# Kernel optimization log

Hardware: AMD Instinct MI355X
Metric: run time of the kernel (lower is better)

Reference implementation:

```python
import jax, jax.numpy as jnp
import numpy as np

N_SRC, N_DST, E = 10000, 40000, 1_280_000
IN_DIM, OUT_DIM, FEAT, O_DIM = 128, 64, 64, 300


def setup_inputs() -> dict:
    key = jax.random.key(0)
    ks = jax.random.split(key, 10)
    s = 0.05
    return {
        "h": jax.random.normal(ks[0], (N_SRC, IN_DIM), jnp.float32),
        "o": jax.random.normal(ks[1], (N_DST, O_DIM), jnp.float32),
        "tfidf": jax.random.normal(ks[2], (E, FEAT), jnp.float32),
        "W_fc": jax.random.normal(ks[3], (IN_DIM, OUT_DIM), jnp.float32) * s,
        "W_fc1": jax.random.normal(ks[4], (O_DIM, OUT_DIM), jnp.float32) * s,
        "W_feat": jax.random.normal(ks[5], (FEAT, OUT_DIM), jnp.float32) * s,
        "b_feat": jax.random.normal(ks[6], (OUT_DIM,), jnp.float32) * s,
        "W_attn": jax.random.normal(ks[7], (OUT_DIM, 1), jnp.float32) * s,
        "edge_src": jax.random.randint(ks[8], (E,), 0, N_SRC, jnp.int32),
        "edge_dst": jax.random.randint(ks[9], (E,), 0, N_DST, jnp.int32),
    }


def reference(h, o, tfidf, W_fc, W_fc1, W_feat, b_feat, W_attn, edge_src, edge_dst):
    n_dst = o.shape[0]
    # node projections: z on sentence (src) nodes via fc, on word (dst) nodes via fc1
    z_src = h @ W_fc                      # [N_SRC, D]
    z_dst = o @ W_fc1                     # [N_DST, D]
    # edge attention: z2 = src.z + dst.z + feat_fc(tfidfembed)
    dfeat = tfidf @ W_feat + b_feat       # [E, D]
    z2 = z_src[edge_src] + z_dst[edge_dst] + dfeat
    z3 = jnp.where(z2 > 0, z2, 0.01 * z2)  # leaky_relu, torch default slope
    e = (z3 @ W_attn)[:, 0]               # [E]
    # segment softmax over incoming edges of each dst (word) node
    m = jax.ops.segment_max(e, edge_dst, num_segments=n_dst)   # [N_DST]
    e_exp = jnp.exp(e - m[edge_dst])                           # [E]
    denom = jax.ops.segment_sum(e_exp, edge_dst, num_segments=n_dst)
    alpha = e_exp / jnp.maximum(denom, 1e-9)[edge_dst]         # [E]
    # weighted sum of src z into dst mailbox
    out = jax.ops.segment_sum(alpha[:, None] * z_src[edge_src], edge_dst,
                              num_segments=n_dst)              # [N_DST, D]
    return out
```

## Files before the change

kernel.cpp:

```cpp
#include <hip/hip_runtime.h>
#include <hip/hip_bf16.h>

#define N_SRC 10000
#define N_DST 40000
#define NE    1280000
#define IN_DIM 128
#define O_DIM  300
#define D      64
#define FEAT   64
#define NB     157

typedef __bf16 bf16x8 __attribute__((ext_vector_type(8)));
typedef __bf16 bf16x4 __attribute__((ext_vector_type(4)));
typedef float  f32x4  __attribute__((ext_vector_type(4)));

__global__ __launch_bounds__(256) void k_zsrc(const float* __restrict__ h,
                                              const float* __restrict__ Wfc,
                                              float* __restrict__ z,
                                              __bf16* __restrict__ zh){
    __shared__ float w[IN_DIM * D];
    for (int i = threadIdx.x; i < IN_DIM * D; i += blockDim.x) w[i] = Wfc[i];
    __syncthreads();
    int lane = threadIdx.x & 63;
    int wid  = blockIdx.x * 4 + (threadIdx.x >> 6);
    int nw   = gridDim.x * 4;
    for (int r0 = wid * 4; r0 < N_SRC; r0 += nw * 4){
        const f32x4* p0 = (const f32x4*)(h + (size_t)(r0 + 0) * IN_DIM);
        const f32x4* p1 = (const f32x4*)(h + (size_t)(r0 + 1) * IN_DIM);
        const f32x4* p2 = (const f32x4*)(h + (size_t)(r0 + 2) * IN_DIM);
        const f32x4* p3 = (const f32x4*)(h + (size_t)(r0 + 3) * IN_DIM);
        float a0 = 0.f, a1 = 0.f, a2 = 0.f, a3 = 0.f;
        #pragma unroll 4
        for (int k4 = 0; k4 < IN_DIM / 4; ++k4){
            f32x4 v0 = p0[k4], v1 = p1[k4], v2 = p2[k4], v3 = p3[k4];
            #pragma unroll
            for (int i = 0; i < 4; ++i){
                float wv = w[(k4 * 4 + i) * D + lane];
                a0 += v0[i] * wv; a1 += v1[i] * wv;
                a2 += v2[i] * wv; a3 += v3[i] * wv;
            }
        }
        z[(size_t)(r0 + 0) * D + lane] = a0; zh[(size_t)(r0 + 0) * D + lane] = (__bf16)a0;
        z[(size_t)(r0 + 1) * D + lane] = a1; zh[(size_t)(r0 + 1) * D + lane] = (__bf16)a1;
        z[(size_t)(r0 + 2) * D + lane] = a2; zh[(size_t)(r0 + 2) * D + lane] = (__bf16)a2;
        z[(size_t)(r0 + 3) * D + lane] = a3; zh[(size_t)(r0 + 3) * D + lane] = (__bf16)a3;
    }
}

__global__ __launch_bounds__(256) void k_zdst(const float* __restrict__ o,
                                              const float* __restrict__ Wfc1,
                                              float* __restrict__ z){
    extern __shared__ float w[];
    for (int i = threadIdx.x; i < O_DIM * D; i += blockDim.x) w[i] = Wfc1[i];
    __syncthreads();
    int lane = threadIdx.x & 63;
    int wid  = blockIdx.x * 4 + (threadIdx.x >> 6);
    int nw   = gridDim.x * 4;
    for (int r0 = wid * 4; r0 < N_DST; r0 += nw * 4){
        const f32x4* p0 = (const f32x4*)(o + (size_t)(r0 + 0) * O_DIM);
        const f32x4* p1 = (const f32x4*)(o + (size_t)(r0 + 1) * O_DIM);
        const f32x4* p2 = (const f32x4*)(o + (size_t)(r0 + 2) * O_DIM);
        const f32x4* p3 = (const f32x4*)(o + (size_t)(r0 + 3) * O_DIM);
        float a0 = 0.f, a1 = 0.f, a2 = 0.f, a3 = 0.f;
        #pragma unroll 5
        for (int k4 = 0; k4 < O_DIM / 4; ++k4){
            f32x4 v0 = p0[k4], v1 = p1[k4], v2 = p2[k4], v3 = p3[k4];
            #pragma unroll
            for (int i = 0; i < 4; ++i){
                float wv = w[(k4 * 4 + i) * D + lane];
                a0 += v0[i] * wv; a1 += v1[i] * wv;
                a2 += v2[i] * wv; a3 += v3[i] * wv;
            }
        }
        z[(size_t)(r0 + 0) * D + lane] = a0;
        z[(size_t)(r0 + 1) * D + lane] = a1;
        z[(size_t)(r0 + 2) * D + lane] = a2;
        z[(size_t)(r0 + 3) * D + lane] = a3;
    }
}

__global__ __launch_bounds__(256) void k_rank(const int* __restrict__ edst,
                                              int* __restrict__ cnt,
                                              int* __restrict__ rank){
    int i = blockIdx.x * blockDim.x + threadIdx.x;
    if (i < NE) rank[i] = atomicAdd(&cnt[edst[i]], 1);
}

__device__ __forceinline__ int block_incl_scan(int c, int* wsum){
    int lane = threadIdx.x & 63, w = threadIdx.x >> 6;
    int v = c;
    #pragma unroll
    for (int off = 1; off < 64; off <<= 1){
        int u = __shfl_up(v, off);
        if (lane >= off) v += u;
    }
    if (lane == 63) wsum[w] = v;
    __syncthreads();
    int add = 0;
    for (int ww = 0; ww < w; ++ww) add += wsum[ww];
    return v + add;
}

__global__ __launch_bounds__(256) void k_scan1(const int* __restrict__ cnt,
                                               int* __restrict__ bsum){
    __shared__ int wsum[4];
    int i = blockIdx.x * 256 + threadIdx.x;
    int c = (i < N_DST) ? cnt[i] : 0;
    int lane = threadIdx.x & 63, w = threadIdx.x >> 6;
    int v = c;
    #pragma unroll
    for (int off = 1; off < 64; off <<= 1) v += __shfl_xor(v, off);
    if (lane == 0) wsum[w] = v;
    __syncthreads();
    if (threadIdx.x == 0)
        bsum[blockIdx.x] = wsum[0] + wsum[1] + wsum[2] + wsum[3];
}

__global__ __launch_bounds__(256) void k_scan2(int* __restrict__ bsum){
    __shared__ int wsum[4];
    int i = threadIdx.x;
    int c = (i < NB) ? bsum[i] : 0;
    int v = block_incl_scan(c, wsum);
    if (i < NB) bsum[i] = v - c;
}

__global__ __launch_bounds__(256) void k_scan3(const int* __restrict__ cnt,
                                               const int* __restrict__ bsum,
                                               int* __restrict__ csr){
    __shared__ int wsum[4];
    int i = blockIdx.x * 256 + threadIdx.x;
    int c = (i < N_DST) ? cnt[i] : 0;
    int v = block_incl_scan(c, wsum);
    int val = bsum[blockIdx.x] + v - c;
    if (i < N_DST) csr[i] = val;
    if (blockIdx.x == 0 && threadIdx.x == 0) csr[N_DST] = NE;
}

__global__ __launch_bounds__(256) void k_edge(
        const float* __restrict__ tfidf,
        const int*   __restrict__ esrc, const int* __restrict__ edst,
        const int*   __restrict__ rank, const int* __restrict__ csr,
        const __bf16* __restrict__ zsrch, const float* __restrict__ zdst,
        const float* __restrict__ Wfeat, const float* __restrict__ bfeat,
        const float* __restrict__ Wattn,
        float* __restrict__ escore_p, int* __restrict__ ssrc_s){
    int lane = threadIdx.x & 63;
    int lo = lane & 15, g = lane >> 4;

    bf16x8 afr[4][2];
    #pragma unroll
    for (int mt = 0; mt < 4; ++mt){
        int m = mt * 16 + lo;
        #pragma unroll
        for (int kh = 0; kh < 2; ++kh){
            #pragma unroll
            for (int j = 0; j < 8; ++j){
                int k = kh * 32 + g * 8 + j;
                afr[mt][kh][j] = (__bf16)Wfeat[k * D + m];
            }
        }
    }
    f32x4 bf4[4], wa4[4];
    #pragma unroll
    for (int mt = 0; mt < 4; ++mt){
        int db = mt * 16 + g * 4;
        bf4[mt] = *(const f32x4*)(bfeat + db);
        wa4[mt] = *(const f32x4*)(Wattn + db);
    }

    const int NT = NE / 16;
    int wid = blockIdx.x * 4 + (threadIdx.x >> 6);
    int nw  = gridDim.x * 4;

    int tile = wid;
    int nss = 0, nsd = 0, npos = 0;
    if (tile < NT){
        int e = tile * 16 + lo;
        nss = esrc[e]; nsd = edst[e];
        npos = csr[nsd] + rank[e];
    }

    for (; tile < NT; tile += nw){
        int css = nss, csd = nsd, cpos = npos;

        bf16x4 zs[4]; f32x4 zd[4];
        #pragma unroll
        for (int mt = 0; mt < 4; ++mt){
            int db = mt * 16 + g * 4;
            zs[mt] = *(const bf16x4*)(zsrch + (size_t)css * D + db);
            zd[mt] = *(const f32x4*)(zdst  + (size_t)csd * D + db);
        }

        int e0 = tile * 16 + lo;
        const float* trow = tfidf + (size_t)e0 * FEAT;
        f32x4 fa0 = __builtin_nontemporal_load((const f32x4*)(trow + g * 8));
        f32x4 fb0 = __builtin_nontemporal_load((const f32x4*)(trow + g * 8 + 4));
        f32x4 fa1 = __builtin_nontemporal_load((const f32x4*)(trow + 32 + g * 8));
        f32x4 fb1 = __builtin_nontemporal_load((const f32x4*)(trow + 32 + g * 8 + 4));

        int tn = tile + nw;
        if (tn < NT){
            int en = tn * 16 + lo;
            nss = esrc[en]; nsd = edst[en];
            npos = csr[nsd] + rank[en];
        }

        bf16x8 bfr[2];
        #pragma unroll
        for (int j = 0; j < 4; ++j){
            bfr[0][j]     = (__bf16)fa0[j];
            bfr[0][4 + j] = (__bf16)fb0[j];
            bfr[1][j]     = (__bf16)fa1[j];
            bfr[1][4 + j] = (__bf16)fb1[j];
        }

        float pacc = 0.f;
        #pragma unroll
        for (int mt = 0; mt < 4; ++mt){
            f32x4 acc = {0.f, 0.f, 0.f, 0.f};
            acc = __builtin_amdgcn_mfma_f32_16x16x32_bf16(afr[mt][0], bfr[0], acc, 0, 0, 0);
            acc = __builtin_amdgcn_mfma_f32_16x16x32_bf16(afr[mt][1], bfr[1], acc, 0, 0, 0);
            #pragma unroll
            for (int r = 0; r < 4; ++r){
                float z2 = acc[r] + (float)zs[mt][r] + zd[mt][r] + bf4[mt][r];
                float z3 = z2 > 0.f ? z2 : 0.01f * z2;
                pacc += z3 * wa4[mt][r];
            }
        }
        pacc += __shfl_xor(pacc, 16);
        pacc += __shfl_xor(pacc, 32);
        if (lane < 16){
            escore_p[cpos] = pacc;
            ssrc_s[cpos]   = css;
        }
    }
}

__global__ __launch_bounds__(256) void k_post(const int* __restrict__ csr,
                                              const int* __restrict__ ssrc,
                                              const float* __restrict__ escore_p,
                                              const float* __restrict__ zsrc,
                                              float* __restrict__ out){
    int lane = threadIdx.x & 63;
    int d    = blockIdx.x * 4 + (threadIdx.x >> 6);
    if (d >= N_DST) return;
    int beg = csr[d], end = csr[d + 1];

    float m = -3.4e38f;
    for (int j = beg + lane; j < end; j += 64)
        m = fmaxf(m, escore_p[j]);
    #pragma unroll
    for (int off = 1; off < 64; off <<= 1)
        m = fmaxf(m, __shfl_xor(m, off));

    float ssum = 0.f;
    for (int j = beg + lane; j < end; j += 64)
        ssum += __expf(escore_p[j] - m);
    #pragma unroll
    for (int off = 1; off < 64; off <<= 1)
        ssum += __shfl_xor(ssum, off);
    float inv = 1.f / fmaxf(ssum, 1e-9f);

    float acc = 0.f;
    for (int base = beg; base < end; base += 64){
        int n = end - base; if (n > 64) n = 64;
        int   sj = 0;
        float aj = 0.f;
        if (base + lane < end){
            sj = ssrc[base + lane];
            aj = __expf(escore_p[base + lane] - m) * inv;
        }
        int t = 0;
        for (; t + 4 <= n; t += 4){
            int   s0 = __shfl(sj, t + 0), s1 = __shfl(sj, t + 1);
            int   s2 = __shfl(sj, t + 2), s3 = __shfl(sj, t + 3);
            float a0 = __shfl(aj, t + 0), a1 = __shfl(aj, t + 1);
            float a2 = __shfl(aj, t + 2), a3 = __shfl(aj, t + 3);
            float v0 = zsrc[(size_t)s0 * D + lane];
            float v1 = zsrc[(size_t)s1 * D + lane];
            float v2 = zsrc[(size_t)s2 * D + lane];
            float v3 = zsrc[(size_t)s3 * D + lane];
            acc += a0 * v0; acc += a1 * v1; acc += a2 * v2; acc += a3 * v3;
        }
        for (; t < n; ++t){
            int   s = __shfl(sj, t);
            float a = __shfl(aj, t);
            acc += a * zsrc[(size_t)s * D + lane];
        }
    }
    out[(size_t)d * D + lane] = acc;
}

extern "C" void kernel_launch(void* const* d_in, const int* in_sizes, int n_in,
                              void* d_out, int out_size, void* d_ws, size_t ws_size,
                              hipStream_t stream) {
    const float* h     = (const float*)d_in[0];
    const float* o     = (const float*)d_in[1];
    const float* tfidf = (const float*)d_in[2];
    const float* Wfc   = (const float*)d_in[3];
    const float* Wfc1  = (const float*)d_in[4];
    const float* Wfeat = (const float*)d_in[5];
    const float* bfeat = (const float*)d_in[6];
    const float* Wattn = (const float*)d_in[7];
    const int*   esrc  = (const int*)d_in[8];
    const int*   edst  = (const int*)d_in[9];
    float* out = (float*)d_out;

    float*  ws      = (float*)d_ws;
    float*  zsrc    = ws;
    float*  zdst    = ws + 640000;
    __bf16* zsrch   = (__bf16*)(ws + 3200000);
    float*  escorep = ws + 3520000;
    int*    ssrc    = (int*)(ws + 4800000);
    int*    rank    = (int*)(ws + 6080000);
    int*    cnt     = (int*)(ws + 7360000);
    int*    csr     = (int*)(ws + 7400000);
    int*    bsum    = (int*)(ws + 7440002);

    hipMemsetAsync(cnt, 0, N_DST * sizeof(int), stream);

    k_zsrc<<<256, 256, 0, stream>>>(h, Wfc, zsrc, zsrch);
    k_zdst<<<512, 256, O_DIM * D * sizeof(float), stream>>>(o, Wfc1, zdst);
    k_rank<<<NE / 256, 256, 0, stream>>>(edst, cnt, rank);
    k_scan1<<<NB, 256, 0, stream>>>(cnt, bsum);
    k_scan2<<<1, 256, 0, stream>>>(bsum);
    k_scan3<<<NB, 256, 0, stream>>>(cnt, bsum, csr);
    k_edge<<<2048, 256, 0, stream>>>(tfidf, esrc, edst, rank, csr, zsrch, zdst,
                                     Wfeat, bfeat, Wattn, escorep, ssrc);
    k_post<<<N_DST / 4, 256, 0, stream>>>(csr, ssrc, escorep, zsrc, out);
}
```

Before: 806.6 us.

## Prefetch tfidf rows one tile ahead, stage Wfeat fragments in LDS, fuse softmax sum pass

The edge kernel now issues the next tile's tfidf loads together with the next index loads, so the large streaming read overlaps the current tile's MFMA work. The index loads are marked nontemporal. The Wfeat MFMA fragments move from registers into a pre-swizzled shared-memory array that is reread each tile, freeing VGPRs at the cost of LDS reads. In the post kernel the separate exp-sum pass is merged into the aggregation loop: unnormalized weights are accumulated and the result is divided at the end, removing one pass over the scores.

```diff
diff --git a/kernel.cpp b/kernel.cpp
--- a/kernel.cpp
+++ b/kernel.cpp
@@ -144,22 +144,18 @@
         const float* __restrict__ Wfeat, const float* __restrict__ bfeat,
         const float* __restrict__ Wattn,
         float* __restrict__ escore_p, int* __restrict__ ssrc_s){
+    __shared__ __bf16 aw[8 * 64 * 8];
+    for (int idx = threadIdx.x; idx < 64 * 64; idx += 256){
+        int k = idx >> 6, m = idx & 63;
+        int kh = k >> 5, r = k & 31, g2 = r >> 3, j = r & 7;
+        int mt = m >> 4, lo2 = m & 15;
+        aw[((((mt << 1) | kh) * 64) + ((g2 << 4) | lo2)) * 8 + j] = (__bf16)Wfeat[idx];
+    }
+    __syncthreads();
+
     int lane = threadIdx.x & 63;
     int lo = lane & 15, g = lane >> 4;
 
-    bf16x8 afr[4][2];
-    #pragma unroll
-    for (int mt = 0; mt < 4; ++mt){
-        int m = mt * 16 + lo;
-        #pragma unroll
-        for (int kh = 0; kh < 2; ++kh){
-            #pragma unroll
-            for (int j = 0; j < 8; ++j){
-                int k = kh * 32 + g * 8 + j;
-                afr[mt][kh][j] = (__bf16)Wfeat[k * D + m];
-            }
-        }
-    }
     f32x4 bf4[4], wa4[4];
     #pragma unroll
     for (int mt = 0; mt < 4; ++mt){
@@ -173,15 +169,25 @@
     int nw  = gridDim.x * 4;
 
     int tile = wid;
-    int nss = 0, nsd = 0, npos = 0;
-    if (tile < NT){
-        int e = tile * 16 + lo;
-        nss = esrc[e]; nsd = edst[e];
-        npos = csr[nsd] + rank[e];
-    }
+    if (tile >= NT) return;
+
+    int e0 = tile * 16 + lo;
+    int nss = __builtin_nontemporal_load(esrc + e0);
+    int nsd = __builtin_nontemporal_load(edst + e0);
+    int nrk = __builtin_nontemporal_load(rank + e0);
+    int npos = csr[nsd] + nrk;
+    {
+        const float* tr = tfidf + (size_t)e0 * FEAT + g * 8;
+    }
+    const float* tr0 = tfidf + (size_t)e0 * FEAT + g * 8;
+    f32x4 nfa0 = __builtin_nontemporal_load((const f32x4*)(tr0));
+    f32x4 nfb0 = __builtin_nontemporal_load((const f32x4*)(tr0 + 4));
+    f32x4 nfa1 = __builtin_nontemporal_load((const f32x4*)(tr0 + 32));
+    f32x4 nfb1 = __builtin_nontemporal_load((const f32x4*)(tr0 + 36));
 
     for (; tile < NT; tile += nw){
         int css = nss, csd = nsd, cpos = npos;
+        f32x4 fa0 = nfa0, fb0 = nfb0, fa1 = nfa1, fb1 = nfb1;
 
         bf16x4 zs[4]; f32x4 zd[4];
         #pragma unroll
@@ -191,18 +197,18 @@
             zd[mt] = *(const f32x4*)(zdst  + (size_t)csd * D + db);
         }
 
-        int e0 = tile * 16 + lo;
-        const float* trow = tfidf + (size_t)e0 * FEAT;
-        f32x4 fa0 = __builtin_nontemporal_load((const f32x4*)(trow + g * 8));
-        f32x4 fb0 = __builtin_nontemporal_load((const f32x4*)(trow + g * 8 + 4));
-        f32x4 fa1 = __builtin_nontemporal_load((const f32x4*)(trow + 32 + g * 8));
-        f32x4 fb1 = __builtin_nontemporal_load((const f32x4*)(trow + 32 + g * 8 + 4));
-
         int tn = tile + nw;
         if (tn < NT){
             int en = tn * 16 + lo;
-            nss = esrc[en]; nsd = edst[en];
-            npos = csr[nsd] + rank[en];
+            nss = __builtin_nontemporal_load(esrc + en);
+            nsd = __builtin_nontemporal_load(edst + en);
+            nrk = __builtin_nontemporal_load(rank + en);
+            npos = csr[nsd] + nrk;
+            const float* trn = tfidf + (size_t)en * FEAT + g * 8;
+            nfa0 = __builtin_nontemporal_load((const f32x4*)(trn));
+            nfb0 = __builtin_nontemporal_load((const f32x4*)(trn + 4));
+            nfa1 = __builtin_nontemporal_load((const f32x4*)(trn + 32));
+            nfb1 = __builtin_nontemporal_load((const f32x4*)(trn + 36));
         }
 
         bf16x8 bfr[2];
@@ -217,9 +223,11 @@
         float pacc = 0.f;
         #pragma unroll
         for (int mt = 0; mt < 4; ++mt){
+            bf16x8 a0 = *(const bf16x8*)(aw + (((mt << 1) | 0) * 64 + lane) * 8);
+            bf16x8 a1 = *(const bf16x8*)(aw + (((mt << 1) | 1) * 64 + lane) * 8);
             f32x4 acc = {0.f, 0.f, 0.f, 0.f};
-            acc = __builtin_amdgcn_mfma_f32_16x16x32_bf16(afr[mt][0], bfr[0], acc, 0, 0, 0);
-            acc = __builtin_amdgcn_mfma_f32_16x16x32_bf16(afr[mt][1], bfr[1], acc, 0, 0, 0);
+            acc = __builtin_amdgcn_mfma_f32_16x16x32_bf16(a0, bfr[0], acc, 0, 0, 0);
+            acc = __builtin_amdgcn_mfma_f32_16x16x32_bf16(a1, bfr[1], acc, 0, 0, 0);
             #pragma unroll
             for (int r = 0; r < 4; ++r){
                 float z2 = acc[r] + (float)zs[mt][r] + zd[mt][r] + bf4[mt][r];
@@ -253,29 +261,22 @@
     for (int off = 1; off < 64; off <<= 1)
         m = fmaxf(m, __shfl_xor(m, off));
 
-    float ssum = 0.f;
-    for (int j = beg + lane; j < end; j += 64)
-        ssum += __expf(escore_p[j] - m);
-    #pragma unroll
-    for (int off = 1; off < 64; off <<= 1)
-        ssum += __shfl_xor(ssum, off);
-    float inv = 1.f / fmaxf(ssum, 1e-9f);
-
-    float acc = 0.f;
+    float ssum = 0.f, acc = 0.f;
     for (int base = beg; base < end; base += 64){
         int n = end - base; if (n > 64) n = 64;
         int   sj = 0;
-        float aj = 0.f;
+        float ej = 0.f;
         if (base + lane < end){
             sj = ssrc[base + lane];
-            aj = __expf(escore_p[base + lane] - m) * inv;
-        }
+            ej = __expf(escore_p[base + lane] - m);
+        }
+        ssum += ej;
         int t = 0;
         for (; t + 4 <= n; t += 4){
             int   s0 = __shfl(sj, t + 0), s1 = __shfl(sj, t + 1);
             int   s2 = __shfl(sj, t + 2), s3 = __shfl(sj, t + 3);
-            float a0 = __shfl(aj, t + 0), a1 = __shfl(aj, t + 1);
-            float a2 = __shfl(aj, t + 2), a3 = __shfl(aj, t + 3);
+            float a0 = __shfl(ej, t + 0), a1 = __shfl(ej, t + 1);
+            float a2 = __shfl(ej, t + 2), a3 = __shfl(ej, t + 3);
             float v0 = zsrc[(size_t)s0 * D + lane];
             float v1 = zsrc[(size_t)s1 * D + lane];
             float v2 = zsrc[(size_t)s2 * D + lane];
@@ -284,11 +285,15 @@
         }
         for (; t < n; ++t){
             int   s = __shfl(sj, t);
-            float a = __shfl(aj, t);
+            float a = __shfl(ej, t);
             acc += a * zsrc[(size_t)s * D + lane];
         }
     }
-    out[(size_t)d * D + lane] = acc;
+    #pragma unroll
+    for (int off = 1; off < 64; off <<= 1)
+        ssum += __shfl_xor(ssum, off);
+    float inv = 1.f / fmaxf(ssum, 1e-9f);
+    out[(size_t)d * D + lane] = acc * inv;
 }
 
 extern "C" void kernel_launch(void* const* d_in, const int* in_sizes, int n_in,
```

Result: no change. 807.0 us (+0.1%).
